# Kernel optimization log

Hardware: AMD Instinct MI355X
Metric: run time of the kernel (lower is better)

## Reference

```python
import jax, jax.numpy as jnp
import numpy as np

PERMS = ((0, 1, 2, 3), (2, 1, 3, 0), (3, 1, 0, 2))


def setup_inputs() -> dict:
    key = jax.random.key(0)
    ks = jax.random.split(key, 10)
    N_n1, F = 50000, 128
    N_imp = 100000
    H = 512
    h = jax.random.normal(ks[0], (N_n1, F), dtype=jnp.float32)
    idx = jax.random.randint(ks[1], (N_imp, 4), 0, N_n1, dtype=jnp.int64)
    s = 0.05
    W1 = jax.random.normal(ks[2], (4 * F, H), dtype=jnp.float32) * s
    b1 = jax.random.normal(ks[3], (H,), dtype=jnp.float32) * s
    W2 = jax.random.normal(ks[4], (H, H), dtype=jnp.float32) * s
    b2 = jax.random.normal(ks[5], (H,), dtype=jnp.float32) * s
    W3 = jax.random.normal(ks[6], (H, H), dtype=jnp.float32) * s
    b3 = jax.random.normal(ks[7], (H,), dtype=jnp.float32) * s
    Wo = jax.random.normal(ks[8], (H, 2), dtype=jnp.float32) * s
    bo = jax.random.normal(ks[9], (2,), dtype=jnp.float32) * s
    return {"h": h, "idx": idx, "W1": W1, "b1": b1, "W2": W2, "b2": b2,
            "W3": W3, "b3": b3, "Wo": Wo, "bo": bo}


def reference(h, idx, W1, b1, W2, b2, W3, b3, Wo, bo):
    # Message passing: copy_u + mean over exactly one edge per relation == gather.
    hi = h[idx]  # [N, 4, F]
    N = hi.shape[0]
    # Stack the 3 permutations of the 4 neighbor features: [3, N, 4F]
    x = jnp.stack([hi[:, jnp.array(p), :].reshape(N, -1) for p in PERMS], axis=0)
    # Shared MLP (config = [512, relu] x 3), broadcast over permutation axis.
    x = jax.nn.relu(x @ W1 + b1)
    x = jax.nn.relu(x @ W2 + b2)
    x = jax.nn.relu(x @ W3 + b3)
    pooled = jnp.sum(x, axis=0)  # Janossy sum over permutations: [N, 512]
    return pooled @ Wo + bo  # [N, 2]
```

## Files before the change

### kernel.cpp

```cpp
#include <hip/hip_runtime.h>
#include <stdint.h>
#include <stddef.h>


typedef __attribute__((ext_vector_type(8))) short short8;
typedef __attribute__((ext_vector_type(16))) float f32x16;
typedef __attribute__((ext_vector_type(4))) float floatv4;
typedef __attribute__((ext_vector_type(8))) unsigned short ushort8;

#define GLOAD_LDS16(g, l)                                                      \
  __builtin_amdgcn_global_load_lds(                                            \
      (const __attribute__((address_space(1))) void*)(g),                      \
      (__attribute__((address_space(3))) void*)(l), 16, 0, 0)

__device__ __forceinline__ unsigned short f2bf(float f) {
  unsigned int u = __float_as_uint(f);
  u += 0x7fffu + ((u >> 16) & 1u);
  return (unsigned short)(u >> 16);
}
__device__ __forceinline__ float bf2f(unsigned short s) {
  return __uint_as_float(((unsigned int)s) << 16);
}

#define NNODES 100000
#define MTOT   300000
#define HD     512
#define NH     50000

__global__ __launch_bounds__(256) void prep_w(const float* __restrict__ W1,
                                              const float* __restrict__ W2,
                                              const float* __restrict__ W3,
                                              unsigned short* __restrict__ Wt) {
  int t = blockIdx.x * 256 + threadIdx.x;
  int layer = t >> 18;
  int r = t & 262143;
  int n = r >> 9, k = r & 511;
  const float* W = layer == 0 ? W1 : (layer == 1 ? W2 : W3);
  Wt[t] = f2bf(W[k * 512 + n]);
}

__global__ __launch_bounds__(256) void prep_hb(const float* __restrict__ h,
                                               unsigned short* __restrict__ hb) {
  int t = blockIdx.x * 256 + threadIdx.x;
  int v = t >> 4, c8 = (t & 15) * 8;
  const floatv4* hp = (const floatv4*)(h + (size_t)v * 128 + c8);
  floatv4 f0 = hp[0], f1 = hp[1];
  ushort8 o;
#pragma unroll
  for (int e = 0; e < 4; ++e) {
    o[e] = f2bf(f0[e]);
    o[4 + e] = f2bf(f1[e]);
  }
  *(ushort8*)(hb + (size_t)v * 128 + c8) = o;
}

__global__ __launch_bounds__(256) void init_out(float* __restrict__ out,
                                                const float* __restrict__ bo) {
  int t = blockIdx.x * 256 + threadIdx.x;
  if (t < 2 * NNODES) out[t] = bo[t & 1];
}

template <int GATHER, int FINAL>
__global__ __launch_bounds__(256, 4) void gemm_k(
    const unsigned short* __restrict__ A,
    const int* __restrict__ idx,
    const unsigned short* __restrict__ Wt,
    const float* __restrict__ bias,
    unsigned short* __restrict__ Xout,
    float* __restrict__ out, const float* __restrict__ Wo,
    int mchunk0) {
  __shared__ __align__(16) char smem[36864];
  char* sA = smem;
  char* sB = smem + 16384;
  int* sIdx = (int*)(smem + 32768);

  const int t = threadIdx.x;
  int bx = blockIdx.x;
  int xcd = bx & 7, tq = bx >> 3;
  int cbk = tq & 3;
  int rb = xcd + ((tq >> 2) << 3);
  int n0 = cbk * 128;
  int arow0 = rb * 128;
  int w = t >> 6, l = t & 63;
  int wm = (w >> 1) * 64, wn = (w & 1) * 64;
  int m32 = l & 31, half = l >> 5;

  if (GATHER) {
    if (t < 128) {
      int m = mchunk0 + arow0 + t;
      unsigned um = (unsigned)m;
      unsigned n = um / 3u;
      int p = (int)(um - n * 3u);
      if (n >= NNODES) n = 0;
      const unsigned pk0 = 0x320u, pk1 = 0x111u, pk2 = 0x032u, pk3 = 0x203u;
      int sh = p * 4;
      sIdx[t * 4 + 0] = idx[n * 4 + ((pk0 >> sh) & 0xFu)];
      sIdx[t * 4 + 1] = idx[n * 4 + ((pk1 >> sh) & 0xFu)];
      sIdx[t * 4 + 2] = idx[n * 4 + ((pk2 >> sh) & 0xFu)];
      sIdx[t * 4 + 3] = idx[n * 4 + ((pk3 >> sh) & 0xFu)];
    }
    __syncthreads();
  }

  f32x16 acc[2][2];
#pragma unroll
  for (int i = 0; i < 2; ++i)
#pragma unroll
    for (int j = 0; j < 2; ++j)
#pragma unroll
      for (int r = 0; r < 16; ++r) acc[i][j][r] = 0.f;

  for (int kt = 0; kt < 8; ++kt) {
    int kb = kt * 64;
    if (GATHER) {
      int jblk = kt >> 1;
      int inner = (kt & 1) * 64;
#pragma unroll
      for (int i = 0; i < 4; ++i) {
        int s = i * 256 + t;
        int r = s >> 3;
        int cl = (s & 7) ^ (r & 7);
        int src = sIdx[r * 4 + jblk];
        GLOAD_LDS16(A + (size_t)src * 128 + inner + cl * 8, sA + s * 16);
      }
    } else {
#pragma unroll
      for (int i = 0; i < 4; ++i) {
        int s = i * 256 + t;
        int r = s >> 3;
        int cl = (s & 7) ^ (r & 7);
        GLOAD_LDS16(A + (size_t)(arow0 + r) * HD + kb + cl * 8, sA + s * 16);
      }
    }
#pragma unroll
    for (int i = 0; i < 4; ++i) {
      int s = i * 256 + t;
      int r = s >> 3;
      int cl = (s & 7) ^ (r & 7);
      GLOAD_LDS16(Wt + (size_t)(n0 + r) * HD + kb + cl * 8, sB + s * 16);
    }
    __syncthreads();
#pragma unroll
    for (int ks = 0; ks < 4; ++ks) {
      short8 af[2], bfr[2];
      int cb = ((ks << 1) + half) ^ (m32 & 7);
#pragma unroll
      for (int i = 0; i < 2; ++i)
        af[i] = *(const short8*)(sA + (wm + i * 32 + m32) * 128 + cb * 16);
#pragma unroll
      for (int j = 0; j < 2; ++j)
        bfr[j] = *(const short8*)(sB + (wn + j * 32 + m32) * 128 + cb * 16);
#pragma unroll
      for (int i = 0; i < 2; ++i)
#pragma unroll
        for (int j = 0; j < 2; ++j)
          acc[i][j] = __builtin_amdgcn_mfma_f32_32x32x16_bf16(af[i], bfr[j],
                                                              acc[i][j], 0, 0, 0);
    }
    __syncthreads();
  }

  unsigned short* L = (unsigned short*)smem;
#pragma unroll
  for (int i = 0; i < 2; ++i)
#pragma unroll
    for (int j = 0; j < 2; ++j) {
      int coll = wn + j * 32 + m32;
      float bv = bias[n0 + coll];
#pragma unroll
      for (int r = 0; r < 16; ++r) {
        int rowl = wm + i * 32 + (r & 3) + 8 * (r >> 2) + 4 * half;
        float v = fmaxf(acc[i][j][r] + bv, 0.f);
        L[rowl * 136 + coll] = f2bf(v);
      }
    }
  __syncthreads();

  if (!FINAL) {
#pragma unroll
    for (int v = 0; v < 8; ++v) {
      int chunk = v * 256 + t;
      int row = chunk >> 4, ch = chunk & 15;
      ushort8 val = *(const ushort8*)(L + row * 136 + ch * 8);
      *(ushort8*)(Xout + (size_t)(arow0 + row) * HD + n0 + ch * 8) = val;
    }
  } else {
    int r2 = t >> 1, jo = t & 1;
    int grow = mchunk0 + arow0 + r2;
    if (grow < MTOT) {
      const unsigned short* Lr = L + r2 * 136;
      float s = 0.f;
#pragma unroll
      for (int cc = 0; cc < 128; cc += 2) {
        unsigned int pair = *(const unsigned int*)(Lr + cc);
        s += bf2f((unsigned short)(pair & 0xffffu)) * Wo[(n0 + cc) * 2 + jo];
        s += bf2f((unsigned short)(pair >> 16)) * Wo[(n0 + cc + 1) * 2 + jo];
      }
      int node = grow / 3;
      atomicAdd(out + node * 2 + jo, s);
    }
  }
}

extern "C" void kernel_launch(void* const* d_in, const int* in_sizes, int n_in,
                              void* d_out, int out_size, void* d_ws,
                              size_t ws_size, hipStream_t stream) {
  const float* h  = (const float*)d_in[0];
  const int*   ix = (const int*)d_in[1];
  const float* W1 = (const float*)d_in[2];
  const float* b1 = (const float*)d_in[3];
  const float* W2 = (const float*)d_in[4];
  const float* b2 = (const float*)d_in[5];
  const float* W3 = (const float*)d_in[6];
  const float* b3 = (const float*)d_in[7];
  const float* Wo = (const float*)d_in[8];
  const float* bo = (const float*)d_in[9];
  float* out = (float*)d_out;

  unsigned short* ws = (unsigned short*)d_ws;
  unsigned short* Wt = ws;
  unsigned short* hb = Wt + 786432;
  unsigned short* bufs = hb + 6400000;
  const size_t baseBytes = (786432ull + 6400000ull) * 2;

  size_t avail = ws_size > baseBytes ? ws_size - baseBytes : 0;
  size_t ncap = avail / (2ull * 3 * HD * sizeof(unsigned short));
  size_t nc = (ncap / 2048) * 2048;
  if (nc > 32768) nc = 32768;
  if (nc == 0) nc = 2048;
  unsigned short* X1 = bufs;
  unsigned short* X2 = X1 + nc * 3 * HD;

  prep_w<<<3072, 256, 0, stream>>>(W1, W2, W3, Wt);
  prep_hb<<<NH * 16 / 256, 256, 0, stream>>>(h, hb);
  init_out<<<(2 * NNODES + 255) / 256, 256, 0, stream>>>(out, bo);

  for (size_t n0c = 0; n0c < NNODES; n0c += nc) {
    size_t remn = (size_t)NNODES - n0c;
    size_t ncp = remn < nc ? ((remn + 2047) / 2048) * 2048 : nc;
    int rows = (int)(ncp * 3);
    int RB = rows / 128;
    int m0 = (int)(3 * n0c);
    gemm_k<1, 0><<<RB * 4, 256, 0, stream>>>(hb, ix, Wt, b1, X1, nullptr,
                                             nullptr, m0);
    gemm_k<0, 0><<<RB * 4, 256, 0, stream>>>(X1, nullptr, Wt + 262144, b2, X2,
                                             nullptr, nullptr, m0);
    gemm_k<0, 1><<<RB * 4, 256, 0, stream>>>(X2, nullptr, Wt + 524288, b3,
                                             nullptr, out, Wo, m0);
  }
}
```

Measured before the change: 700.9 us.

## Store activations and weights in MFMA-fragment tiled layout for contiguous LDS loads

Weights and intermediate activations are now written in a pre-tiled layout that matches the MFMA operand order. Each 128x64 k-tile becomes one contiguous 16KB block, so global-to-LDS loads are fully linear and fragment reads are conflict-free without the XOR swizzle. The epilogue LDS stride changes to 152, and the final layer caches its Wo slice in shared memory instead of reading it from global memory. The cost is a more complex index mapping in prep_w and the writeback, plus slightly more LDS per block.

```diff
diff --git a/kernel.cpp b/kernel.cpp
--- a/kernel.cpp
+++ b/kernel.cpp
@@ -26,6 +26,7 @@
 #define MTOT   300000
 #define HD     512
 #define NH     50000
+#define LSTR   152
 
 __global__ __launch_bounds__(256) void prep_w(const float* __restrict__ W1,
                                               const float* __restrict__ W2,
@@ -34,7 +35,15 @@
   int t = blockIdx.x * 256 + threadIdx.x;
   int layer = t >> 18;
   int r = t & 262143;
-  int n = r >> 9, k = r & 511;
+  int e = r & 7;
+  int q16 = r >> 3;
+  int s = q16 & 1023;
+  int blk = q16 >> 10;
+  int nb = blk >> 3, kt = blk & 7;
+  int c = ((s >> 8) << 1) | ((s >> 5) & 1);
+  int row = ((s >> 6) & 3) * 32 + (s & 31);
+  int n = nb * 128 + row;
+  int k = kt * 64 + c * 8 + e;
   const float* W = layer == 0 ? W1 : (layer == 1 ? W2 : W3);
   Wt[t] = f2bf(W[k * 512 + n]);
 }
@@ -69,10 +78,11 @@
     unsigned short* __restrict__ Xout,
     float* __restrict__ out, const float* __restrict__ Wo,
     int mchunk0) {
-  __shared__ __align__(16) char smem[36864];
+  __shared__ __align__(16) char smem[39936];
   char* sA = smem;
   char* sB = smem + 16384;
   int* sIdx = (int*)(smem + 32768);
+  float* sWo = (float*)(smem + 38912);
 
   const int t = threadIdx.x;
   int bx = blockIdx.x;
@@ -80,14 +90,14 @@
   int cbk = tq & 3;
   int rb = xcd + ((tq >> 2) << 3);
   int n0 = cbk * 128;
-  int arow0 = rb * 128;
+  int rb8 = rb * 8;
   int w = t >> 6, l = t & 63;
-  int wm = (w >> 1) * 64, wn = (w & 1) * 64;
+  int wmq = (w >> 1) * 2, wnq = (w & 1) * 2;
   int m32 = l & 31, half = l >> 5;
 
   if (GATHER) {
     if (t < 128) {
-      int m = mchunk0 + arow0 + t;
+      int m = mchunk0 + rb * 128 + t;
       unsigned um = (unsigned)m;
       unsigned n = um / 3u;
       int p = (int)(um - n * 3u);
@@ -111,45 +121,40 @@
       for (int r = 0; r < 16; ++r) acc[i][j][r] = 0.f;
 
   for (int kt = 0; kt < 8; ++kt) {
-    int kb = kt * 64;
     if (GATHER) {
-      int jblk = kt >> 1;
-      int inner = (kt & 1) * 64;
+      int jn = kt >> 1;
+      int base = (kt & 1) * 64;
+      int row = ((t >> 6) & 3) * 32 + (t & 31);
+      int src = sIdx[row * 4 + jn];
+      int hbit = (t >> 5) & 1;
 #pragma unroll
       for (int i = 0; i < 4; ++i) {
-        int s = i * 256 + t;
-        int r = s >> 3;
-        int cl = (s & 7) ^ (r & 7);
-        int src = sIdx[r * 4 + jblk];
-        GLOAD_LDS16(A + (size_t)src * 128 + inner + cl * 8, sA + s * 16);
+        int c = (i << 1) | hbit;
+        GLOAD_LDS16(A + (size_t)src * 128 + base + c * 8,
+                    sA + (i * 256 + t) * 16);
       }
     } else {
-#pragma unroll
-      for (int i = 0; i < 4; ++i) {
-        int s = i * 256 + t;
-        int r = s >> 3;
-        int cl = (s & 7) ^ (r & 7);
-        GLOAD_LDS16(A + (size_t)(arow0 + r) * HD + kb + cl * 8, sA + s * 16);
-      }
-    }
-#pragma unroll
-    for (int i = 0; i < 4; ++i) {
-      int s = i * 256 + t;
-      int r = s >> 3;
-      int cl = (s & 7) ^ (r & 7);
-      GLOAD_LDS16(Wt + (size_t)(n0 + r) * HD + kb + cl * 8, sB + s * 16);
+      const unsigned short* ga = A + ((size_t)(rb8 + kt) * 1024 + t) * 8;
+#pragma unroll
+      for (int i = 0; i < 4; ++i)
+        GLOAD_LDS16(ga + (size_t)i * 2048, sA + (i * 256 + t) * 16);
+    }
+    {
+      const unsigned short* gb = Wt + ((size_t)(cbk * 8 + kt) * 1024 + t) * 8;
+#pragma unroll
+      for (int i = 0; i < 4; ++i)
+        GLOAD_LDS16(gb + (size_t)i * 2048, sB + (i * 256 + t) * 16);
     }
     __syncthreads();
 #pragma unroll
     for (int ks = 0; ks < 4; ++ks) {
       short8 af[2], bfr[2];
-      int cb = ((ks << 1) + half) ^ (m32 & 7);
 #pragma unroll
       for (int i = 0; i < 2; ++i)
-        af[i] = *(const short8*)(sA + (wm + i * 32 + m32) * 128 + cb * 16);
+        af[i] = *(const short8*)(sA + (ks * 256 + (wmq + i) * 64 + l) * 16);
 #pragma unroll
       for (int j = 0; j < 2; ++j)
-        bfr[j] = *(const short8*)(sB + (wn + j * 32 + m32) * 128 + cb * 16);
+        bfr[j] = *(const short8*)(sB + (ks * 256 + (wnq + j) * 64 + l) * 16);
 #pragma unroll
       for (int i = 0; i < 2; ++i)
 #pragma unroll
@@ -161,17 +166,18 @@
   }
 
   unsigned short* L = (unsigned short*)smem;
+  if (FINAL && t < 256) sWo[t] = Wo[n0 * 2 + t];
 #pragma unroll
   for (int i = 0; i < 2; ++i)
 #pragma unroll
     for (int j = 0; j < 2; ++j) {
-      int coll = wn + j * 32 + m32;
+      int coll = wnq * 32 + j * 32 + m32;
       float bv = bias[n0 + coll];
 #pragma unroll
       for (int r = 0; r < 16; ++r) {
-        int rowl = wm + i * 32 + (r & 3) + 8 * (r >> 2) + 4 * half;
+        int rowl = wmq * 32 + i * 32 + (r & 3) + 8 * (r >> 2) + 4 * half;
         float v = fmaxf(acc[i][j][r] + bv, 0.f);
-        L[rowl * 136 + coll] = f2bf(v);
+        L[rowl * LSTR + coll] = f2bf(v);
       }
     }
   __syncthreads();
@@ -180,21 +186,27 @@
 #pragma unroll
     for (int v = 0; v < 8; ++v) {
       int chunk = v * 256 + t;
-      int row = chunk >> 4, ch = chunk & 15;
-      ushort8 val = *(const ushort8*)(L + row * 136 + ch * 8);
-      *(ushort8*)(Xout + (size_t)(arow0 + row) * HD + n0 + ch * 8) = val;
+      int ktsel = chunk >> 10;
+      int s = chunk & 1023;
+      int ks_l = s >> 8;
+      int rowhi = (s >> 6) & 3;
+      int hb_ = (s >> 5) & 1;
+      int row = rowhi * 32 + (s & 31);
+      int col_local = ktsel * 64 + (((ks_l << 1) | hb_) << 3);
+      ushort8 val = *(const ushort8*)(L + row * LSTR + col_local);
+      *(ushort8*)(Xout + ((size_t)(rb8 + 2 * cbk + ktsel) * 1024 + s) * 8) = val;
     }
   } else {
     int r2 = t >> 1, jo = t & 1;
-    int grow = mchunk0 + arow0 + r2;
+    int grow = mchunk0 + rb * 128 + r2;
     if (grow < MTOT) {
-      const unsigned short* Lr = L + r2 * 136;
+      const unsigned short* Lr = L + r2 * LSTR;
       float s = 0.f;
 #pragma unroll
       for (int cc = 0; cc < 128; cc += 2) {
         unsigned int pair = *(const unsigned int*)(Lr + cc);
-        s += bf2f((unsigned short)(pair & 0xffffu)) * Wo[(n0 + cc) * 2 + jo];
-        s += bf2f((unsigned short)(pair >> 16)) * Wo[(n0 + cc + 1) * 2 + jo];
+        s += bf2f((unsigned short)(pair & 0xffffu)) * sWo[2 * cc + jo];
+        s += bf2f((unsigned short)(pair >> 16)) * sWo[2 * cc + 2 + jo];
       }
       int node = grow / 3;
       atomicAdd(out + node * 2 + jo, s);
```

New measurement: 733.5 us. 1.05x slower.
